# Kernel optimization log

Hardware: AMD Instinct MI355X
Metric: run time of the kernel (lower is better)

The kernel has to match this reference:

```python
import jax, jax.numpy as jnp
import numpy as np

H = 64  # hidden_size
IN = 6  # input_size


def _uniform(key, shape, bound):
    return jax.random.uniform(key, shape, jnp.float32, -bound, bound)


def setup_inputs() -> dict:
    key = jax.random.key(0)
    ks = jax.random.split(key, 20)
    B, T = 1024, 512
    bnd = 1.0 / np.sqrt(H)  # PyTorch LSTM/Linear default init scale
    inp = {"x": jax.random.normal(ks[0], (B, T, IN), jnp.float32)}
    # LSTM params, PyTorch layout: w_ih [4H, in], w_hh [4H, H], gate order i,f,g,o
    in_sizes = [IN, H, H]
    for l in range(3):
        inp[f"w_ih{l}"] = _uniform(ks[1 + 4 * l], (4 * H, in_sizes[l]), bnd)
        inp[f"w_hh{l}"] = _uniform(ks[2 + 4 * l], (4 * H, H), bnd)
        inp[f"b_ih{l}"] = _uniform(ks[3 + 4 * l], (4 * H,), bnd)
        inp[f"b_hh{l}"] = _uniform(ks[4 + 4 * l], (4 * H,), bnd)
    # MLP head: fc1 (64->128), fc3 (128->64), fc2 (64->2)
    inp["fc1_w"] = _uniform(ks[13], (128, H), 1.0 / np.sqrt(H))
    inp["fc1_b"] = _uniform(ks[14], (128,), 1.0 / np.sqrt(H))
    inp["fc3_w"] = _uniform(ks[15], (64, 128), 1.0 / np.sqrt(128))
    inp["fc3_b"] = _uniform(ks[16], (64,), 1.0 / np.sqrt(128))
    inp["fc2_w"] = _uniform(ks[17], (2, 64), 1.0 / np.sqrt(64))
    inp["fc2_b"] = _uniform(ks[18], (2,), 1.0 / np.sqrt(64))
    return inp


def _lstm_layer(x, w_ih, w_hh, b_ih, b_hh):
    # x: [B, T, F] -> [B, T, H]; zero initial state, PyTorch gate order i,f,g,o
    B = x.shape[0]
    # Precompute input projections for all timesteps (one big GEMM)
    xg = jnp.einsum('btf,gf->btg', x, w_ih) + b_ih + b_hh  # [B, T, 4H]

    def step(carry, xt):
        h, c = carry
        gates = xt + h @ w_hh.T
        i, f, g, o = jnp.split(gates, 4, axis=-1)
        c = jax.nn.sigmoid(f) * c + jax.nn.sigmoid(i) * jnp.tanh(g)
        h = jax.nn.sigmoid(o) * jnp.tanh(c)
        return (h, c), h

    h0 = jnp.zeros((B, H), x.dtype)
    (_, _), ys = jax.lax.scan(step, (h0, h0), jnp.swapaxes(xg, 0, 1))
    return jnp.swapaxes(ys, 0, 1)


def reference(x, w_ih0, w_hh0, b_ih0, b_hh0, w_ih1, w_hh1, b_ih1, b_hh1,
              w_ih2, w_hh2, b_ih2, b_hh2, fc1_w, fc1_b, fc3_w, fc3_b, fc2_w, fc2_b):
    h = _lstm_layer(x, w_ih0, w_hh0, b_ih0, b_hh0)
    h = _lstm_layer(h, w_ih1, w_hh1, b_ih1, b_hh1)
    h = _lstm_layer(h, w_ih2, w_hh2, b_ih2, b_hh2)
    z = h[:, -1, :]  # last timestep: [B, H]
    z = jax.nn.relu(z @ fc1_w.T + fc1_b)
    z = jax.nn.relu(z @ fc3_w.T + fc3_b)
    return z @ fc2_w.T + fc2_b  # [B, 2]
```

## Files before the change

### kernel.cpp

```cpp
#include <hip/hip_runtime.h>
#include <cstdint>
#include <cstddef>

namespace {

constexpr int B_ = 1024;
constexpr int T_ = 512;
constexpr int H_ = 64;
constexpr int NG = 64;
constexpr int D_RING = 64;
constexpr int CP = 16;
constexpr int SLOT_BYTES = 16 * 64 * 2;

constexpr float L2E  = 1.4426950408889634f;

typedef short bf16x8 __attribute__((ext_vector_type(8)));
typedef float f32x4  __attribute__((ext_vector_type(4)));

__device__ __forceinline__ float exp2_hw(float x) {
    float r; asm("v_exp_f32 %0, %1" : "=v"(r) : "v"(x)); return r;
}
__device__ __forceinline__ float rcp_hw(float x) {
    float r; asm("v_rcp_f32 %0, %1" : "=v"(r) : "v"(x)); return r;
}

__device__ __forceinline__ unsigned short f2bf(float f) {
    unsigned u = __float_as_uint(f);
    u += 0x7FFF + ((u >> 16) & 1);
    return (unsigned short)(u >> 16);
}

__device__ __forceinline__ unsigned cvtpk_bf16(float a, float b) {
    unsigned r;
    asm("v_cvt_pk_bf16_f32 %0, %1, %2" : "=v"(r) : "v"(a), "v"(b));
    return r;
}

__device__ __forceinline__ void lds_barrier() {
    asm volatile("s_waitcnt lgkmcnt(0)\n\ts_barrier" ::: "memory");
}

__device__ __forceinline__ void ring_store16(void* dst, bf16x8 v) {
    asm volatile("global_store_dwordx4 %0, %1, off sc0 sc1"
                 :: "v"(dst), "v"(v) : "memory");
}
__device__ __forceinline__ int flag_load(const int* p) {
    int v;
    asm volatile("global_load_dword %0, %1, off sc0 sc1\n\t"
                 "s_waitcnt vmcnt(0)" : "=v"(v) : "v"(p) : "memory");
    return v;
}
__device__ __forceinline__ void flag_store_drain(int* p, int v) {
    asm volatile("s_waitcnt vmcnt(0)\n\t"
                 "global_store_dword %0, %1, off sc0 sc1"
                 :: "v"(p), "v"(v) : "memory");
}
__device__ __forceinline__ void flag_store(int* p, int v) {
    asm volatile("global_store_dword %0, %1, off sc0 sc1"
                 :: "v"(p), "v"(v) : "memory");
}
__device__ __forceinline__ void spin_ge(const int* p, int tgt) {
    while (flag_load(p) < tgt) __builtin_amdgcn_s_sleep(1);
}

template<int R>
__device__ __forceinline__ float cell_one(const f32x4* accC, float& cr) {
    const float gi = accC[0][R], gf = accC[1][R], gg = accC[2][R], go = accC[3][R];
    const float A  = exp2_hw(-gi);
    const float F  = exp2_hw(-gf);
    const float Bx = exp2_hw(-gg);
    const float D  = exp2_hw(-go);
    const float r1 = rcp_hw((1.0f + A) * (1.0f + Bx));
    const float r2 = rcp_hw(1.0f + F);
    cr = __builtin_fmaf(cr, r2, (1.0f - Bx) * r1);
    float ca = cr * (-2.0f * L2E);
    ca = fminf(fmaxf(ca, -80.0f), 80.0f);
    const float C  = exp2_hw(ca);
    const float r3 = rcp_hw((1.0f + D) * (1.0f + C));
    return (1.0f - C) * r3;
}

__global__ void init_flags(int* p, int n) {
    int i = blockIdx.x * 256 + threadIdx.x;
    if (i < n) p[i] = -1;
}

__global__ void cvt_bf16_kernel(const float* __restrict__ src,
                                unsigned short* __restrict__ dst, int n) {
    int i = blockIdx.x * 256 + threadIdx.x;
    if (i < n) {
        int row = i >> 6;
        float sc = ((row >> 6) == 2) ? 2.0f * L2E : L2E;
        dst[i] = f2bf(src[i] * sc);
    }
}

__global__ void cvt_wih0_kernel(const float* __restrict__ src,
                                unsigned short* __restrict__ dst) {
    int i = blockIdx.x * 256 + threadIdx.x;
    int g = i >> 3, k = i & 7;
    float sc = ((g >> 6) == 2) ? 2.0f * L2E : L2E;
    dst[i] = (k < 6) ? f2bf(src[g * 6 + k] * sc) : (unsigned short)0;
}

__global__ void build_xpk(const float* __restrict__ x,
                          unsigned short* __restrict__ xPk) {
    int idx = blockIdx.x * 256 + threadIdx.x;
    int k = idx & 7, r = (idx >> 3) & 15, g = (idx >> 7) & 63, t = idx >> 13;
    float v = (k < 6) ? x[((size_t)(g * 16 + r) * T_ + t) * 6 + k] : 0.f;
    xPk[idx] = f2bf(v);
}

template<int LAY>
__device__ __forceinline__ void pipe_body(
    int g,
    const unsigned short* __restrict__ xPk,
    const unsigned short* __restrict__ wih,
    const unsigned short* __restrict__ whh,
    const float* __restrict__ bih, const float* __restrict__ bhh,
    const unsigned short* __restrict__ ringIn, unsigned short* __restrict__ ringOut,
    const int* progIn, int* progOut, int* consInP, const int* consOutP,
    float* __restrict__ hlast, unsigned short* lds)
{
    const int tid = threadIdx.x;
    const int l   = tid & 63;
    const int w   = tid >> 6;
    const int r16 = l & 15;
    const int kq  = l >> 4;
    const int hdim = w * 16 + r16;

    bf16x8 whh_f[4][2], wih_f[4][2];
    f32x4  bias_acc[4];
    #pragma unroll
    for (int d = 0; d < 4; ++d) {
        const int gg = d * 64 + hdim;
        const float sc = (d == 2) ? 2.0f * L2E : L2E;
        const float b = (bih[gg] + bhh[gg]) * sc;
        bias_acc[d] = f32x4{b, b, b, b};
        whh_f[d][0] = *(const bf16x8*)(whh + gg * 64 + kq * 8);
        whh_f[d][1] = *(const bf16x8*)(whh + gg * 64 + 32 + kq * 8);
        if constexpr (LAY == 0) {
            bf16x8 z = {};
            wih_f[d][0] = (kq == 0) ? *(const bf16x8*)(wih + gg * 8) : z;
            wih_f[d][1] = z;
        } else {
            wih_f[d][0] = *(const bf16x8*)(wih + gg * 64 + kq * 8);
            wih_f[d][1] = *(const bf16x8*)(wih + gg * 64 + 32 + kq * 8);
        }
    }

    char* ldsb = (char*)lds;
    const int rdA0 = r16 * 128 + (((0 + kq) ^ (r16 & 7)) << 4);
    const int rdA1 = r16 * 128 + (((4 + kq) ^ (r16 & 7)) << 4);
    int wrA[4];
    #pragma unroll
    for (int r = 0; r < 4; ++r) {
        const int row = 4 * kq + r;
        wrA[r] = row * 128 + (((hdim >> 3) ^ (row & 7)) << 4) + (hdim & 7) * 2;
    }
    const int rOffA = r16 * 128 + kq * 16;
    const int rOffB = r16 * 128 + 64 + kq * 16;

    auto xrow = [&](int t) -> const char* {
        return (const char*)xPk + (((size_t)t * NG + g) * 16 + r16) * 16;
    };

    ((uint4*)ldsb)[tid] = make_uint4(0, 0, 0, 0);
    float c[4] = {0.f, 0.f, 0.f, 0.f};
    lds_barrier();

    bf16x8 cur0 = {};
    bf16x8 curA0 = {}, curA1 = {};
    bf16x8 curB0 = {}, curB1 = {};
    f32x4 accA[4], accB[4];
    {
        bf16x8 x0a = {}, x0b = {};
        if constexpr (LAY > 0) {
            spin_ge(progIn, (CP - 1 < T_ - 1) ? CP - 1 : T_ - 1);
            const char* s0 = (const char*)ringIn;
            const char* s1 = (const char*)ringIn + SLOT_BYTES;
            const char* s2 = (const char*)ringIn + 2 * SLOT_BYTES;
            asm volatile(
                "global_load_dwordx4 %0, %6, off sc0 sc1\n\t"
                "global_load_dwordx4 %1, %7, off sc0 sc1\n\t"
                "global_load_dwordx4 %2, %8, off sc0 sc1\n\t"
                "global_load_dwordx4 %3, %9, off sc0 sc1\n\t"
                "global_load_dwordx4 %4, %10, off sc0 sc1\n\t"
                "global_load_dwordx4 %5, %11, off sc0 sc1\n\t"
                "s_waitcnt vmcnt(0)"
                : "=v"(x0a), "=v"(x0b), "=v"(curA0), "=v"(curA1),
                  "=v"(curB0), "=v"(curB1)
                : "v"(s0 + rOffA), "v"(s0 + rOffB),
                  "v"(s1 + rOffA), "v"(s1 + rOffB),
                  "v"(s2 + rOffA), "v"(s2 + rOffB)
                : "memory");
            __builtin_amdgcn_sched_barrier(0);
        } else {
            asm volatile(
                "global_load_dwordx4 %0, %2, off\n\t"
                "global_load_dwordx4 %1, %3, off\n\t"
                "s_waitcnt vmcnt(0)"
                : "=v"(x0a), "=v"(cur0)
                : "v"(xrow(0)), "v"(xrow(1))
                : "memory");
            __builtin_amdgcn_sched_barrier(0);
        }
        #pragma unroll
        for (int d = 0; d < 4; ++d) {
            accA[d] = __builtin_amdgcn_mfma_f32_16x16x32_bf16(x0a, wih_f[d][0], bias_acc[d], 0, 0, 0);
            if constexpr (LAY != 0)
                accA[d] = __builtin_amdgcn_mfma_f32_16x16x32_bf16(x0b, wih_f[d][1], accA[d], 0, 0, 0);
        }
    }

    auto step = [&](int t, int par, bool tail, f32x4* accC, f32x4* accN,
                    bf16x8& cp0, bf16x8& cp1) {
        if constexpr (LAY < 2) {
            if (w == 0 && (t & (CP - 1)) == 0) spin_ge(consOutP, t + CP - D_RING);
        }

        const bf16x8 ha = *(const bf16x8*)(ldsb + ((par ^ 1) << 11) + rdA0);
        const bf16x8 hb = *(const bf16x8*)(ldsb + ((par ^ 1) << 11) + rdA1);

        #pragma unroll
        for (int d = 0; d < 4; ++d) {
            accC[d] = __builtin_amdgcn_mfma_f32_16x16x32_bf16(ha, whh_f[d][0], accC[d], 0, 0, 0);
            accC[d] = __builtin_amdgcn_mfma_f32_16x16x32_bf16(hb, whh_f[d][1], accC[d], 0, 0, 0);
        }

        if (tail) {
            asm volatile("s_waitcnt vmcnt(0)" ::: "memory");
        } else if constexpr (LAY == 0) {
            if (w == 0) asm volatile("s_waitcnt vmcnt(2)" ::: "memory");
            else        asm volatile("s_waitcnt vmcnt(0)" ::: "memory");
        } else if constexpr (LAY == 1) {
            if (w == 0) asm volatile("s_waitcnt vmcnt(7)" ::: "memory");
            else        asm volatile("s_waitcnt vmcnt(2)" ::: "memory");
        } else {
            asm volatile("s_waitcnt vmcnt(2)" ::: "memory");
        }
        __builtin_amdgcn_sched_barrier(0);

        if constexpr (LAY == 0) {
            if (tid == 0) flag_store(progOut, t - 3);
        } else if constexpr (LAY == 1) {
            if (tid == 0) flag_store(progOut, t - 4);
        }

        if (t + 1 < T_) {
            if constexpr (LAY == 0) {
                #pragma unroll
                for (int d = 0; d < 4; ++d)
                    accN[d] = __builtin_amdgcn_mfma_f32_16x16x32_bf16(cur0, wih_f[d][0], bias_acc[d], 0, 0, 0);
            } else {
                #pragma unroll
                for (int d = 0; d < 4; ++d) {
                    accN[d] = __builtin_amdgcn_mfma_f32_16x16x32_bf16(cp0, wih_f[d][0], bias_acc[d], 0, 0, 0);
                    accN[d] = __builtin_amdgcn_mfma_f32_16x16x32_bf16(cp1, wih_f[d][1], accN[d], 0, 0, 0);
                }
            }
        }

        {
            const int s = (LAY > 0) ? t + 3 : t + 2;
            if (s < T_) {
                if constexpr (LAY > 0) {
                    if ((s & (CP - 1)) == 0) {
                        int tgt = s + CP - 1; if (tgt > T_ - 1) tgt = T_ - 1;
                        spin_ge(progIn, tgt);
                    }
                    const char* src = (const char*)ringIn + (s & (D_RING - 1)) * SLOT_BYTES;
                    asm volatile(
                        "global_load_dwordx4 %0, %2, off sc0 sc1\n\t"
                        "global_load_dwordx4 %1, %3, off sc0 sc1"
                        : "=v"(cp0), "=v"(cp1)
                        : "v"(src + rOffA), "v"(src + rOffB)
                        : "memory");
                } else {
                    asm volatile("global_load_dwordx4 %0, %1, off"
                                 : "=v"(cur0) : "v"(xrow(s)) : "memory");
                }
            }
        }

        if constexpr (LAY < 2) {
            if (w == 0) {
                char* dst = (char*)ringOut + ((t - 1) & (D_RING - 1)) * SLOT_BYTES;
                ring_store16(dst + rOffA, ha);
                ring_store16(dst + rOffB, hb);
            }
        }

        float h[4];
        h[0] = cell_one<0>(accC, c[0]);
        h[1] = cell_one<1>(accC, c[1]);
        h[2] = cell_one<2>(accC, c[2]);
        h[3] = cell_one<3>(accC, c[3]);
        const unsigned p01 = cvtpk_bf16(h[0], h[1]);
        const unsigned p23 = cvtpk_bf16(h[2], h[3]);
        char* wbase = ldsb + (par << 11);
        *(unsigned short*)(wbase + wrA[0]) = (unsigned short)(p01 & 0xffff);
        *(unsigned short*)(wbase + wrA[1]) = (unsigned short)(p01 >> 16);
        *(unsigned short*)(wbase + wrA[2]) = (unsigned short)(p23 & 0xffff);
        *(unsigned short*)(wbase + wrA[3]) = (unsigned short)(p23 >> 16);
        if constexpr (LAY == 2) {
            if (t == T_ - 1) {
                #pragma unroll
                for (int r = 0; r < 4; ++r)
                    hlast[(g * 16 + kq * 4 + r) * 64 + hdim] = h[r];
            }
        }

        lds_barrier();

        if constexpr (LAY > 0) {
            if (tid == 0 && (t & (CP - 1)) == CP - 1) flag_store(consInP, t);
        }
    };

    #pragma unroll 1
    for (int t = 0; t < T_ - 4; t += 2) {
        step(t,     0, false, accA, accB, curA0, curA1);
        step(t + 1, 1, false, accB, accA, curB0, curB1);
    }
    step(T_ - 4, 0, true, accA, accB, curA0, curA1);
    step(T_ - 3, 1, true, accB, accA, curB0, curB1);
    step(T_ - 2, 0, true, accA, accB, curA0, curA1);
    step(T_ - 1, 1, true, accB, accA, curB0, curB1);

    if constexpr (LAY < 2) {
        if (w == 0) {
            const int par = (T_ - 1) & 1;
            const bf16x8 ha = *(const bf16x8*)(ldsb + (par << 11) + rdA0);
            const bf16x8 hb = *(const bf16x8*)(ldsb + (par << 11) + rdA1);
            char* dst = (char*)ringOut + ((T_ - 1) & (D_RING - 1)) * SLOT_BYTES;
            ring_store16(dst + rOffA, ha);
            ring_store16(dst + rOffB, hb);
        }
        lds_barrier();
        if (tid == 0) flag_store_drain(progOut, T_ - 1);
    }
}

__global__ __launch_bounds__(256, 1)
void lstm_pipe(const unsigned short* __restrict__ xPk,
               const unsigned short* __restrict__ wih0p,
               const unsigned short* __restrict__ wih1,
               const unsigned short* __restrict__ wih2,
               const unsigned short* __restrict__ whh0,
               const unsigned short* __restrict__ whh1,
               const unsigned short* __restrict__ whh2,
               const float* __restrict__ bih0, const float* __restrict__ bhh0,
               const float* __restrict__ bih1, const float* __restrict__ bhh1,
               const float* __restrict__ bih2, const float* __restrict__ bhh2,
               unsigned short* __restrict__ ring, int* __restrict__ flags,
               float* __restrict__ hlast)
{
    __shared__ unsigned short lds[2][1024];

    const int g   = blockIdx.x & 63;
    const int lay = blockIdx.x >> 6;

    const size_t GSHORTS = (size_t)D_RING * SLOT_BYTES / 2;
    unsigned short* r0 = ring + ((size_t)0 * NG + g) * GSHORTS;
    unsigned short* r1 = ring + ((size_t)1 * NG + g) * GSHORTS;
    int* prog0 = flags + (0 * 64 + g) * 16;
    int* prog1 = flags + (1 * 64 + g) * 16;
    int* cons0 = flags + (128 + 0 * 64 + g) * 16;
    int* cons1 = flags + (128 + 1 * 64 + g) * 16;

    if (lay == 0) {
        pipe_body<0>(g, xPk, wih0p, whh0, bih0, bhh0,
                     nullptr, r0, nullptr, prog0, nullptr, cons0,
                     hlast, &lds[0][0]);
    } else if (lay == 1) {
        pipe_body<1>(g, xPk, wih1, whh1, bih1, bhh1,
                     r0, r1, prog0, prog1, cons0, cons1,
                     hlast, &lds[0][0]);
    } else {
        pipe_body<2>(g, xPk, wih2, whh2, bih2, bhh2,
                     r1, nullptr, prog1, nullptr, cons1, nullptr,
                     hlast, &lds[0][0]);
    }
}

__global__ __launch_bounds__(128)
void mlp_head_kernel(const float* __restrict__ hlast,
                     const float* __restrict__ fc1_w, const float* __restrict__ fc1_b,
                     const float* __restrict__ fc3_w, const float* __restrict__ fc3_b,
                     const float* __restrict__ fc2_w, const float* __restrict__ fc2_b,
                     float* __restrict__ outp)
{
    __shared__ float s_h[H_];
    __shared__ float s_z1[128];
    __shared__ float s_z3[64];
    const int b = blockIdx.x, tid = threadIdx.x;

    if (tid < H_) s_h[tid] = hlast[b * H_ + tid];
    __syncthreads();

    {
        float acc = fc1_b[tid];
        #pragma unroll
        for (int k = 0; k < H_; ++k) acc += fc1_w[tid * H_ + k] * s_h[k];
        s_z1[tid] = fmaxf(acc, 0.0f);
    }
    __syncthreads();

    if (tid < 64) {
        float acc = fc3_b[tid];
        #pragma unroll
        for (int k = 0; k < 128; ++k) acc += fc3_w[tid * 128 + k] * s_z1[k];
        s_z3[tid] = fmaxf(acc, 0.0f);
    }
    __syncthreads();

    if (tid < 2) {
        float acc = fc2_b[tid];
        #pragma unroll
        for (int k = 0; k < 64; ++k) acc += fc2_w[tid * 64 + k] * s_z3[k];
        outp[b * 2 + tid] = acc;
    }
}

}

extern "C" void kernel_launch(void* const* d_in, const int* in_sizes, int n_in,
                              void* d_out, int out_size, void* d_ws, size_t ws_size,
                              hipStream_t stream) {
    (void)in_sizes; (void)n_in; (void)out_size; (void)ws_size;

    const float* x     = (const float*)d_in[0];
    const float* wih0  = (const float*)d_in[1];
    const float* whh0  = (const float*)d_in[2];
    const float* bih0  = (const float*)d_in[3];
    const float* bhh0  = (const float*)d_in[4];
    const float* wih1  = (const float*)d_in[5];
    const float* whh1  = (const float*)d_in[6];
    const float* bih1  = (const float*)d_in[7];
    const float* bhh1  = (const float*)d_in[8];
    const float* wih2  = (const float*)d_in[9];
    const float* whh2  = (const float*)d_in[10];
    const float* bih2  = (const float*)d_in[11];
    const float* bhh2  = (const float*)d_in[12];
    const float* fc1_w = (const float*)d_in[13];
    const float* fc1_b = (const float*)d_in[14];
    const float* fc3_w = (const float*)d_in[15];
    const float* fc3_b = (const float*)d_in[16];
    const float* fc2_w = (const float*)d_in[17];
    const float* fc2_b = (const float*)d_in[18];
    float* out = (float*)d_out;

    char* base = (char*)d_ws;
    const size_t RING_B = (size_t)2 * NG * D_RING * SLOT_BYTES;
    const size_t XPK_B  = (size_t)T_ * NG * 16 * 8 * 2;
    const size_t FLAG_B = 4096 * sizeof(int);
    unsigned short* ring  = (unsigned short*)(base);
    unsigned short* xPk   = (unsigned short*)(base + RING_B);
    int*            flags = (int*)(base + RING_B + XPK_B);
    float*          hlast = (float*)(base + RING_B + XPK_B + FLAG_B);
    char* wp = base + RING_B + XPK_B + FLAG_B + (size_t)B_ * H_ * 4;
    unsigned short* whh_b[3];
    for (int i = 0; i < 3; ++i) { whh_b[i] = (unsigned short*)wp; wp += 256 * 64 * 2; }
    unsigned short* wih_b1 = (unsigned short*)wp; wp += 256 * 64 * 2;
    unsigned short* wih_b2 = (unsigned short*)wp; wp += 256 * 64 * 2;
    unsigned short* wih0p  = (unsigned short*)wp; wp += 256 * 8 * 2;

    init_flags<<<16, 256, 0, stream>>>(flags, 4096);
    const int NW = 256 * 64;
    cvt_bf16_kernel<<<NW / 256, 256, 0, stream>>>(whh0, whh_b[0], NW);
    cvt_bf16_kernel<<<NW / 256, 256, 0, stream>>>(whh1, whh_b[1], NW);
    cvt_bf16_kernel<<<NW / 256, 256, 0, stream>>>(whh2, whh_b[2], NW);
    cvt_bf16_kernel<<<NW / 256, 256, 0, stream>>>(wih1, wih_b1, NW);
    cvt_bf16_kernel<<<NW / 256, 256, 0, stream>>>(wih2, wih_b2, NW);
    cvt_wih0_kernel<<<8, 256, 0, stream>>>(wih0, wih0p);
    build_xpk<<<(T_ * NG * 16 * 8) / 256, 256, 0, stream>>>(x, xPk);

    lstm_pipe<<<192, 256, 0, stream>>>(xPk, wih0p, wih_b1, wih_b2,
                                       whh_b[0], whh_b[1], whh_b[2],
                                       bih0, bhh0, bih1, bhh1, bih2, bhh2,
                                       ring, flags, hlast);

    mlp_head_kernel<<<B_, 128, 0, stream>>>(hlast, fc1_w, fc1_b, fc3_w, fc3_b,
                                            fc2_w, fc2_b, out);
}
```

Before: 380.6 us.

## Fuse setup kernels, read raw x in layer 0, batch progress flag stores

Replaces the seven small setup launches (flag init, weight conversions, x packing) with one combined setup kernel. Drops the separate x pre-packing pass, so layer 0 loads fp32 x directly with three dwordx2 loads per step and converts to bf16 in-register. Progress flags for layers 0 and 1 are now published once every CP steps with a draining store, not on every step, and the vmcnt waits are adjusted to match. This trims launch overhead and a full pass over x in exchange for more conversion work in the recurrent loop and coarser producer/consumer signaling, which may delay downstream layers.

```diff
diff --git a/kernel.cpp b/kernel.cpp
--- a/kernel.cpp
+++ b/kernel.cpp
@@ -16,6 +16,7 @@
 
 typedef short bf16x8 __attribute__((ext_vector_type(8)));
 typedef float f32x4  __attribute__((ext_vector_type(4)));
+typedef float f32x2  __attribute__((ext_vector_type(2)));
 
 __device__ __forceinline__ float exp2_hw(float x) {
     float r; asm("v_exp_f32 %0, %1" : "=v"(r) : "v"(x)); return r;
@@ -33,6 +34,14 @@
 __device__ __forceinline__ unsigned cvtpk_bf16(float a, float b) {
     unsigned r;
     asm("v_cvt_pk_bf16_f32 %0, %1, %2" : "=v"(r) : "v"(a), "v"(b));
+    return r;
+}
+
+__device__ __forceinline__ bf16x8 cvt_x6(f32x2 a, f32x2 b, f32x2 c) {
+    bf16x8 r = {};
+    r[0] = (short)f2bf(a[0]); r[1] = (short)f2bf(a[1]);
+    r[2] = (short)f2bf(b[0]); r[3] = (short)f2bf(b[1]);
+    r[4] = (short)f2bf(c[0]); r[5] = (short)f2bf(c[1]);
     return r;
 }
 
@@ -80,41 +89,45 @@
     return (1.0f - C) * r3;
 }
 
-__global__ void init_flags(int* p, int n) {
-    int i = blockIdx.x * 256 + threadIdx.x;
-    if (i < n) p[i] = -1;
-}
-
-__global__ void cvt_bf16_kernel(const float* __restrict__ src,
-                                unsigned short* __restrict__ dst, int n) {
-    int i = blockIdx.x * 256 + threadIdx.x;
-    if (i < n) {
-        int row = i >> 6;
-        float sc = ((row >> 6) == 2) ? 2.0f * L2E : L2E;
-        dst[i] = f2bf(src[i] * sc);
-    }
-}
-
-__global__ void cvt_wih0_kernel(const float* __restrict__ src,
-                                unsigned short* __restrict__ dst) {
-    int i = blockIdx.x * 256 + threadIdx.x;
-    int g = i >> 3, k = i & 7;
-    float sc = ((g >> 6) == 2) ? 2.0f * L2E : L2E;
-    dst[i] = (k < 6) ? f2bf(src[g * 6 + k] * sc) : (unsigned short)0;
-}
-
-__global__ void build_xpk(const float* __restrict__ x,
-                          unsigned short* __restrict__ xPk) {
-    int idx = blockIdx.x * 256 + threadIdx.x;
-    int k = idx & 7, r = (idx >> 3) & 15, g = (idx >> 7) & 63, t = idx >> 13;
-    float v = (k < 6) ? x[((size_t)(g * 16 + r) * T_ + t) * 6 + k] : 0.f;
-    xPk[idx] = f2bf(v);
+__global__ void setup_all(const float* __restrict__ whh0,
+                          const float* __restrict__ whh1,
+                          const float* __restrict__ whh2,
+                          const float* __restrict__ wih1,
+                          const float* __restrict__ wih2,
+                          const float* __restrict__ wih0,
+                          unsigned short* __restrict__ whhb0,
+                          unsigned short* __restrict__ whhb1,
+                          unsigned short* __restrict__ whhb2,
+                          unsigned short* __restrict__ wihb1,
+                          unsigned short* __restrict__ wihb2,
+                          unsigned short* __restrict__ wih0p,
+                          int* __restrict__ flags)
+{
+    const int i = blockIdx.x * 256 + threadIdx.x;
+    if (i < 81920) {
+        const int which = i >> 14;
+        const int rem   = i & 16383;
+        const float* src = (which == 0) ? whh0 : (which == 1) ? whh1 :
+                           (which == 2) ? whh2 : (which == 3) ? wih1 : wih2;
+        unsigned short* dst = (which == 0) ? whhb0 : (which == 1) ? whhb1 :
+                              (which == 2) ? whhb2 : (which == 3) ? wihb1 : wihb2;
+        const int row = rem >> 6;
+        const float sc = ((row >> 6) == 2) ? 2.0f * L2E : L2E;
+        dst[rem] = f2bf(src[rem] * sc);
+    } else if (i < 83968) {
+        const int j = i - 81920;
+        const int gte = j >> 3, k = j & 7;
+        const float sc = ((gte >> 6) == 2) ? 2.0f * L2E : L2E;
+        wih0p[j] = (k < 6) ? f2bf(wih0[gte * 6 + k] * sc) : (unsigned short)0;
+    } else if (i < 88064) {
+        flags[i - 83968] = -1;
+    }
 }
 
 template<int LAY>
 __device__ __forceinline__ void pipe_body(
     int g,
-    const unsigned short* __restrict__ xPk,
+    const float* __restrict__ xraw,
     const unsigned short* __restrict__ wih,
     const unsigned short* __restrict__ whh,
     const float* __restrict__ bih, const float* __restrict__ bhh,
@@ -161,15 +174,15 @@
     const int rOffA = r16 * 128 + kq * 16;
     const int rOffB = r16 * 128 + 64 + kq * 16;
 
-    auto xrow = [&](int t) -> const char* {
-        return (const char*)xPk + (((size_t)t * NG + g) * 16 + r16) * 16;
+    auto xaddr = [&](int t) -> const char* {
+        return (const char*)xraw + ((size_t)(g * 16 + r16) * T_ + t) * 24;
     };
 
     ((uint4*)ldsb)[tid] = make_uint4(0, 0, 0, 0);
     float c[4] = {0.f, 0.f, 0.f, 0.f};
     lds_barrier();
 
-    bf16x8 cur0 = {};
+    f32x2  xf0 = {}, xf1 = {}, xf2 = {};
     bf16x8 curA0 = {}, curA1 = {};
     bf16x8 curB0 = {}, curB1 = {};
     f32x4 accA[4], accB[4];
@@ -196,14 +209,22 @@
                 : "memory");
             __builtin_amdgcn_sched_barrier(0);
         } else {
+            f32x2 a0 = {}, a1 = {}, a2 = {};
             asm volatile(
-                "global_load_dwordx4 %0, %2, off\n\t"
-                "global_load_dwordx4 %1, %3, off\n\t"
+                "global_load_dwordx2 %0, %6, off\n\t"
+                "global_load_dwordx2 %1, %7, off\n\t"
+                "global_load_dwordx2 %2, %8, off\n\t"
+                "global_load_dwordx2 %3, %9, off\n\t"
+                "global_load_dwordx2 %4, %10, off\n\t"
+                "global_load_dwordx2 %5, %11, off\n\t"
                 "s_waitcnt vmcnt(0)"
-                : "=v"(x0a), "=v"(cur0)
-                : "v"(xrow(0)), "v"(xrow(1))
+                : "=v"(a0), "=v"(a1), "=v"(a2),
+                  "=v"(xf0), "=v"(xf1), "=v"(xf2)
+                : "v"(xaddr(0)), "v"(xaddr(0) + 8), "v"(xaddr(0) + 16),
+                  "v"(xaddr(1)), "v"(xaddr(1) + 8), "v"(xaddr(1) + 16)
                 : "memory");
             __builtin_amdgcn_sched_barrier(0);
+            x0a = cvt_x6(a0, a1, a2);
         }
         #pragma unroll
         for (int d = 0; d < 4; ++d) {
@@ -217,6 +238,11 @@
                     bf16x8& cp0, bf16x8& cp1) {
         if constexpr (LAY < 2) {
             if (w == 0 && (t & (CP - 1)) == 0) spin_ge(consOutP, t + CP - D_RING);
+        }
+        if constexpr (LAY < 2) {
+            if ((t & (CP - 1)) == 1 && t > 1) {
+                if (tid == 0) flag_store_drain(progOut, t - 2);
+            }
         }
 
         const bf16x8 ha = *(const bf16x8*)(ldsb + ((par ^ 1) << 11) + rdA0);
@@ -234,24 +260,19 @@
             if (w == 0) asm volatile("s_waitcnt vmcnt(2)" ::: "memory");
             else        asm volatile("s_waitcnt vmcnt(0)" ::: "memory");
         } else if constexpr (LAY == 1) {
-            if (w == 0) asm volatile("s_waitcnt vmcnt(7)" ::: "memory");
+            if (w == 0) asm volatile("s_waitcnt vmcnt(6)" ::: "memory");
             else        asm volatile("s_waitcnt vmcnt(2)" ::: "memory");
         } else {
             asm volatile("s_waitcnt vmcnt(2)" ::: "memory");
         }
         __builtin_amdgcn_sched_barrier(0);
 
-        if constexpr (LAY == 0) {
-            if (tid == 0) flag_store(progOut, t - 3);
-        } else if constexpr (LAY == 1) {
-            if (tid == 0) flag_store(progOut, t - 4);
-        }
-
         if (t + 1 < T_) {
             if constexpr (LAY == 0) {
+                const bf16x8 xc = cvt_x6(xf0, xf1, xf2);
                 #pragma unroll
                 for (int d = 0; d < 4; ++d)
-                    accN[d] = __builtin_amdgcn_mfma_f32_16x16x32_bf16(cur0, wih_f[d][0], bias_acc[d], 0, 0, 0);
+                    accN[d] = __builtin_amdgcn_mfma_f32_16x16x32_bf16(xc, wih_f[d][0], bias_acc[d], 0, 0, 0);
             } else {
                 #pragma unroll
                 for (int d = 0; d < 4; ++d) {
@@ -277,8 +298,13 @@
                         : "v"(src + rOffA), "v"(src + rOffB)
                         : "memory");
                 } else {
-                    asm volatile("global_load_dwordx4 %0, %1, off"
-                                 : "=v"(cur0) : "v"(xrow(s)) : "memory");
+                    asm volatile(
+                        "global_load_dwordx2 %0, %3, off\n\t"
+                        "global_load_dwordx2 %1, %4, off\n\t"
+                        "global_load_dwordx2 %2, %5, off"
+                        : "=v"(xf0), "=v"(xf1), "=v"(xf2)
+                        : "v"(xaddr(s)), "v"(xaddr(s) + 8), "v"(xaddr(s) + 16)
+                        : "memory");
                 }
             }
         }
@@ -343,7 +369,7 @@
 }
 
 __global__ __launch_bounds__(256, 1)
-void lstm_pipe(const unsigned short* __restrict__ xPk,
+void lstm_pipe(const float* __restrict__ xraw,
                const unsigned short* __restrict__ wih0p,
                const unsigned short* __restrict__ wih1,
                const unsigned short* __restrict__ wih2,
@@ -370,15 +396,15 @@
     int* cons1 = flags + (128 + 1 * 64 + g) * 16;
 
     if (lay == 0) {
-        pipe_body<0>(g, xPk, wih0p, whh0, bih0, bhh0,
+        pipe_body<0>(g, xraw, wih0p, whh0, bih0, bhh0,
                      nullptr, r0, nullptr, prog0, nullptr, cons0,
                      hlast, &lds[0][0]);
     } else if (lay == 1) {
-        pipe_body<1>(g, xPk, wih1, whh1, bih1, bhh1,
+        pipe_body<1>(g, nullptr, wih1, whh1, bih1, bhh1,
                      r0, r1, prog0, prog1, cons0, cons1,
                      hlast, &lds[0][0]);
     } else {
-        pipe_body<2>(g, xPk, wih2, whh2, bih2, bhh2,
+        pipe_body<2>(g, nullptr, wih2, whh2, bih2, bhh2,
                      r1, nullptr, prog1, nullptr, cons1, nullptr,
                      hlast, &lds[0][0]);
     }
@@ -453,30 +479,22 @@
 
     char* base = (char*)d_ws;
     const size_t RING_B = (size_t)2 * NG * D_RING * SLOT_BYTES;
-    const size_t XPK_B  = (size_t)T_ * NG * 16 * 8 * 2;
     const size_t FLAG_B = 4096 * sizeof(int);
     unsigned short* ring  = (unsigned short*)(base);
-    unsigned short* xPk   = (unsigned short*)(base + RING_B);
-    int*            flags = (int*)(base + RING_B + XPK_B);
-    float*          hlast = (float*)(base + RING_B + XPK_B + FLAG_B);
-    char* wp = base + RING_B + XPK_B + FLAG_B + (size_t)B_ * H_ * 4;
+    int*            flags = (int*)(base + RING_B);
+    float*          hlast = (float*)(base + RING_B + FLAG_B);
+    char* wp = base + RING_B + FLAG_B + (size_t)B_ * H_ * 4;
     unsigned short* whh_b[3];
     for (int i = 0; i < 3; ++i) { whh_b[i] = (unsigned short*)wp; wp += 256 * 64 * 2; }
     unsigned short* wih_b1 = (unsigned short*)wp; wp += 256 * 64 * 2;
     unsigned short* wih_b2 = (unsigned short*)wp; wp += 256 * 64 * 2;
     unsigned short* wih0p  = (unsigned short*)wp; wp += 256 * 8 * 2;
 
-    init_flags<<<16, 256, 0, stream>>>(flags, 4096);
-    const int NW = 256 * 64;
-    cvt_bf16_kernel<<<NW / 256, 256, 0, stream>>>(whh0, whh_b[0], NW);
-    cvt_bf16_kernel<<<NW / 256, 256, 0, stream>>>(whh1, whh_b[1], NW);
-    cvt_bf16_kernel<<<NW / 256, 256, 0, stream>>>(whh2, whh_b[2], NW);
-    cvt_bf16_kernel<<<NW / 256, 256, 0, stream>>>(wih1, wih_b1, NW);
-    cvt_bf16_kernel<<<NW / 256, 256, 0, stream>>>(wih2, wih_b2, NW);
-    cvt_wih0_kernel<<<8, 256, 0, stream>>>(wih0, wih0p);
-    build_xpk<<<(T_ * NG * 16 * 8) / 256, 256, 0, stream>>>(x, xPk);
-
-    lstm_pipe<<<192, 256, 0, stream>>>(xPk, wih0p, wih_b1, wih_b2,
+    setup_all<<<344, 256, 0, stream>>>(whh0, whh1, whh2, wih1, wih2, wih0,
+                                       whh_b[0], whh_b[1], whh_b[2],
+                                       wih_b1, wih_b2, wih0p, flags);
+
+    lstm_pipe<<<192, 256, 0, stream>>>(x, wih0p, wih_b1, wih_b2,
                                        whh_b[0], whh_b[1], whh_b[2],
                                        bih0, bhh0, bih1, bhh1, bih2, bhh2,
                                        ring, flags, hlast);
```

Measured after the change: 366.8 us. -3.6%, faster.
